# Kernel optimization log

Hardware: AMD Instinct MI355X
Metric: run time of the kernel (lower is better)

Reference implementation:

```python
import jax, jax.numpy as jnp
import numpy as np

BN_EPS = 1e-5


def binarize(x):
    # sign binarization with straight-through estimator (identity grad)
    return x + jax.lax.stop_gradient(jnp.sign(x) - x)


def conv2d(x, w, stride):
    # x: [N,C,H,W], w: [O,I,kh,kw], VALID padding (PyTorch default padding=0)
    return jax.lax.conv_general_dilated(
        x, w, window_strides=(stride, stride), padding='VALID',
        dimension_numbers=('NCHW', 'OIHW', 'NCHW'))


def batchnorm(x, gamma, beta, mean, var):
    inv = gamma / jnp.sqrt(var + BN_EPS)          # [C]
    return x * inv[None, :, None, None] + (beta - mean * inv)[None, :, None, None]


def setup_inputs() -> dict:
    key = jax.random.key(0)
    ks = jax.random.split(key, 20)
    B = 8192
    f32 = jnp.float32
    d = {
        'x': jax.random.normal(ks[0], (B, 1, 24, 54), f32),
        'conv1_w': jax.random.normal(ks[1], (32, 1, 3, 3), f32) * 0.3,
        'conv1_b': jax.random.normal(ks[2], (32,), f32) * 0.1,
        'bn1_gamma': 1.0 + 0.1 * jax.random.normal(ks[3], (32,), f32),
        'bn1_beta': 0.1 * jax.random.normal(ks[4], (32,), f32),
        'bn1_mean': 0.1 * jax.random.normal(ks[5], (32,), f32),
        'bn1_var': jax.random.uniform(ks[6], (32,), f32, 0.5, 1.5),
        'conv2_w': jax.random.normal(ks[7], (64, 32, 3, 3), f32) * 0.1,
        'conv2_b': jax.random.normal(ks[8], (64,), f32) * 0.1,
        'bn2_gamma': 1.0 + 0.1 * jax.random.normal(ks[9], (64,), f32),
        'bn2_beta': 0.1 * jax.random.normal(ks[10], (64,), f32),
        'bn2_mean': 0.1 * jax.random.normal(ks[11], (64,), f32),
        'bn2_var': jax.random.uniform(ks[12], (64,), f32, 0.5, 1.5),
        'lin_w': jax.random.normal(ks[13], (500, 3840), f32) * 0.02,
        'lin_b': jax.random.normal(ks[14], (500,), f32) * 0.1,
        'out_w': jax.random.normal(ks[15], (10, 500), f32) * 0.05,
        'out_b': jax.random.normal(ks[16], (10,), f32) * 0.1,
    }
    return d


def reference(x, conv1_w, conv1_b, bn1_gamma, bn1_beta, bn1_mean, bn1_var,
              conv2_w, conv2_b, bn2_gamma, bn2_beta, bn2_mean, bn2_var,
              lin_w, lin_b, out_w, out_b):
    # conv1: input channels (1) != 3 -> input binarized; weight binarized; float bias
    h = conv2d(binarize(x), binarize(conv1_w), 2) + conv1_b[None, :, None, None]
    h = jax.nn.relu(batchnorm(h, bn1_gamma, bn1_beta, bn1_mean, bn1_var))  # [B,32,11,26]
    # conv2: input channels (32) != 3 -> input binarized (values in {0,1} post-ReLU)
    h = conv2d(binarize(h), binarize(conv2_w), 2) + conv2_b[None, :, None, None]
    h = jax.nn.relu(batchnorm(h, bn2_gamma, bn2_beta, bn2_mean, bn2_var))  # [B,64,5,12]
    h = h.reshape(-1, 3840)
    # BinarizeLinear: in_features (3840, 500) != 784 -> input binarized
    h = jax.nn.relu(binarize(h) @ binarize(lin_w).T + lin_b[None, :])      # [B,500]
    y = binarize(h) @ binarize(out_w).T + out_b[None, :]                   # [B,10]
    return y
```

## Files before the change

### kernel.cpp

```cpp
#include <hip/hip_runtime.h>
#include <cstdint>

#define BN_EPS 1e-5f

static constexpr int NB = 8192;
static constexpr int JLIN = 500;


__global__ __launch_bounds__(256) void pack_kernel(
    const float* __restrict__ conv1_w, const float* __restrict__ conv1_b,
    const float* __restrict__ conv2_w, const float* __restrict__ conv2_b,
    const float* __restrict__ lin_w, const float* __restrict__ lin_b,
    const float* __restrict__ out_w,
    const float* __restrict__ bn1_g, const float* __restrict__ bn1_b,
    const float* __restrict__ bn1_m, const float* __restrict__ bn1_v,
    const float* __restrict__ bn2_g, const float* __restrict__ bn2_b,
    const float* __restrict__ bn2_m, const float* __restrict__ bn2_v,
    uint32_t* __restrict__ wlin4, uint32_t* __restrict__ cdat,
    uint32_t* __restrict__ lut, uint32_t* __restrict__ wout,
    int* __restrict__ Tlin)
{
    __shared__ uint32_t s_bm[122];
    __shared__ float    s_c1w[288];
    __shared__ uint32_t s_wp[32];
    __shared__ float    s_inv1[32], s_sh1[32], s_b1[32];

    int tid  = threadIdx.x;
    int lane = tid & 63;
    int wv   = tid >> 6;
    int b    = blockIdx.x;

    if (b < 500) {
        int j = b;
        if (tid == 0) { s_bm[120] = 0; s_bm[121] = 0; }
        for (int it = 0; it < 15; ++it) {
            int i = it * 256 + tid;
            float v = lin_w[(size_t)j * 3840 + i];
            uint64_t mask = __ballot(v > 0.0f);
            if (lane == 0)
                *((uint64_t*)&s_bm[(it * 256 + wv * 64) >> 5]) = mask;
        }
        __syncthreads();
        if (tid < 128) {
            int k = tid;
            int c = k >> 1, hi = k & 1;
            int nb = hi ? 28 : 32;
            int f0 = c * 60 + hi * 32;
            uint32_t lo  = s_bm[f0 >> 5];
            uint32_t hiw = s_bm[(f0 >> 5) + 1];
            int sh = f0 & 31;
            uint32_t word = (uint32_t)((((uint64_t)hiw << 32) | lo) >> sh);
            if (nb < 32) word &= (1u << nb) - 1u;
            int jw = j >> 6, jl = j & 63, kq = k >> 2, q = k & 3;
            wlin4[jw * 8192 + kq * 256 + jl * 4 + q] = word;
        }
        return;
    }

    int mb = b - 500;
    if (mb < 2) {
        for (int i = tid; i < 288; i += 256) s_c1w[i] = conv1_w[i];
        __syncthreads();
        if (tid < 32) {
            uint32_t wp = 0;
            for (int t = 0; t < 9; ++t)
                wp |= (s_c1w[tid * 9 + t] < 0.0f ? 1u : 0u) << t;
            s_wp[tid] = wp;
            float inv = bn1_g[tid] / sqrtf(bn1_v[tid] + BN_EPS);
            s_inv1[tid] = inv;
            s_sh1[tid]  = bn1_b[tid] - bn1_m[tid] * inv;
            s_b1[tid]   = conv1_b[tid];
        }
        __syncthreads();
        uint32_t px = (uint32_t)(mb * 256 + tid);
        uint32_t word = 0;
        for (int c = 0; c < 32; ++c) {
            int d = 9 - 2 * __popc(px ^ s_wp[c]);
            float z = __fadd_rn((float)d, s_b1[c]);
            z = __fadd_rn(__fmul_rn(z, s_inv1[c]), s_sh1[c]);
            word |= (z > 0.0f ? 1u : 0u) << c;
        }
        lut[px] = word;
        return;
    }

    int idx = (mb - 2) * 256 + tid;
    if (idx < 576) {
        int c = idx / 9, tap = idx % 9;
        uint32_t w = 0;
        for (int ic = 0; ic < 32; ++ic)
            w |= (conv2_w[c * 288 + ic * 9 + tap] > 0.0f ? 1u : 0u) << ic;
        float inv = bn2_g[c] / sqrtf(bn2_v[c] + BN_EPS);
        if (inv < 0.0f) w = ~w;
        cdat[tap * 64 + c] = w;
    } else if (idx < 576 + 64) {
        int c = idx - 576;
        float inv = bn2_g[c] / sqrtf(bn2_v[c] + BN_EPS);
        float sh  = bn2_b[c] - bn2_m[c] * inv;
        float b2  = conv2_b[c];
        int T = 10000;
        for (int u = -300; u <= 300; ++u) {
            float v = (inv < 0.0f) ? (float)(-u) : (float)u;
            float z = __fadd_rn(__fmul_rn(__fadd_rn(v, b2), inv), sh);
            if (z > 0.0f) { T = u; break; }
        }
        cdat[576 + c] = (uint32_t)T;
    } else if (idx < 576 + 64 + 512) {
        int j = idx - (576 + 64);
        int T = 10000;
        if (j < JLIN) {
            float lb = lin_b[j];
            int base = (int)floorf(-lb) - 2;
            for (int u = base; u <= base + 5; ++u)
                if (__fadd_rn((float)u, lb) > 0.0f) { T = u; break; }
        }
        Tlin[j] = T;
    } else if (idx < 576 + 64 + 512 + 160) {
        int t = idx - (576 + 64 + 512);
        int j = t >> 4, k = t & 15;
        uint32_t w = 0;
        for (int bb = 0; bb < 32; ++bb) {
            int jj = k * 32 + bb;
            if (jj < JLIN) w |= (out_w[j * 500 + jj] > 0.0f ? 1u : 0u) << bb;
        }
        wout[t] = w;
    }
}

__global__ __launch_bounds__(256) void conv_kernel(
    const float* __restrict__ x,
    const uint32_t* __restrict__ cdat,
    const uint32_t* __restrict__ lut,
    uint32_t* __restrict__ h2b, int* __restrict__ Bs)
{
    __shared__ __align__(8) uint32_t s_flat[4][44];
    __shared__ uint32_t s_lut[512];
    __shared__ __align__(8) uint32_t s_in[4][288];
    __shared__ uint32_t s_base[4][64];

    int tid  = threadIdx.x;
    int lane = tid & 63;
    int wv   = tid >> 6;
    int s    = blockIdx.x * 4 + wv;

    s_lut[tid]       = lut[tid];
    s_lut[tid + 256] = lut[tid + 256];

    const float* xs = x + (size_t)s * 1296;
    #pragma unroll
    for (int it = 0; it < 21; ++it) {
        int f = it * 64 + lane;
        float v = (f < 1296) ? xs[f] : 1.0f;
        uint64_t mk = __ballot(v < 0.0f);
        if (lane == 0) *((uint64_t*)&s_flat[wv][2 * it]) = mk;
    }
    __syncthreads();

    for (int i = tid; i < 4 * 286; i += 256) {
        int sl = i / 286, p = i - sl * 286;
        int oy = p / 26, ox = p - oy * 26;
        uint32_t pxb = 0;
        #pragma unroll
        for (int ky = 0; ky < 3; ++ky) {
            int bitpos = 54 * (2 * oy + ky) + 2 * ox;
            int d  = bitpos >> 5;
            int sh = bitpos & 31;
            uint64_t wp = (uint64_t)s_flat[sl][d] | ((uint64_t)s_flat[sl][d + 1] << 32);
            pxb |= (((uint32_t)(wp >> sh)) & 7u) << (3 * ky);
        }
        s_in[sl][p] = s_lut[pxb];
    }
    __syncthreads();

    for (int i = tid; i < 4 * 60; i += 256) {
        int sl = i / 60, p = i - sl * 60;
        int oy = p / 12, ox = p - 12 * oy;
        uint32_t sum = 0;
        #pragma unroll
        for (int ky = 0; ky < 3; ++ky) {
            const uint32_t* rp = &s_in[sl][(2 * oy + ky) * 26 + 2 * ox];
            sum += __popc(rp[0]) + __popc(rp[1]) + __popc(rp[2]);
        }
        s_base[sl][p] = sum;
    }
    __syncthreads();

    int c = lane;
    uint32_t m[9];
    #pragma unroll
    for (int q = 0; q < 9; ++q) m[q] = cdat[q * 64 + c];
    int T = (int)cdat[576 + c];

    uint64_t acc = 0;
    for (int oy = 0; oy < 5; ++oy) {
        int P[12];
        #pragma unroll
        for (int ox = 0; ox < 12; ++ox) P[ox] = 0;
        #pragma unroll
        for (int ky = 0; ky < 3; ++ky) {
            const uint32_t* rp = &s_in[wv][(2 * oy + ky) * 26];
            uint32_t r[25];
            #pragma unroll
            for (int d = 0; d < 12; ++d)
                *(uint64_t*)&r[2 * d] = *(const uint64_t*)&rp[2 * d];
            r[24] = rp[24];
            uint32_t m0 = m[ky * 3 + 0], m1 = m[ky * 3 + 1], m2 = m[ky * 3 + 2];
            #pragma unroll
            for (int ox = 0; ox < 12; ++ox) {
                P[ox] += __popc(r[2 * ox]     & m0);
                P[ox] += __popc(r[2 * ox + 1] & m1);
                P[ox] += __popc(r[2 * ox + 2] & m2);
            }
        }
        const uint32_t* bp = &s_base[wv][oy * 12];
        uint32_t bits = 0;
        #pragma unroll
        for (int ox = 0; ox < 12; ++ox) {
            int v = 2 * P[ox] - (int)bp[ox];
            bits |= (v >= T ? 1u : 0u) << ox;
        }
        acc |= (uint64_t)bits << (12 * oy);
    }
    uint32_t w0 = (uint32_t)acc;
    uint32_t w1 = (uint32_t)(acc >> 32) & 0x0FFFFFFFu;

    int bsum = __popc(w0) + __popc(w1);
    #pragma unroll
    for (int off = 32; off > 0; off >>= 1) bsum += __shfl_xor(bsum, off, 64);
    if (lane == 0) Bs[s] = bsum;

    *(uint2*)(h2b + (size_t)s * 128 + 2 * c) = make_uint2(w0, w1);
}

__global__ __launch_bounds__(256) void lin_kernel(
    const uint32_t* __restrict__ h2b,
    const uint32_t* __restrict__ wlin4,
    const int* __restrict__ Tlin,
    const int* __restrict__ Bs,
    const uint32_t* __restrict__ wout,
    const float* __restrict__ out_b,
    float* __restrict__ out)
{
    __shared__ uint4    s_w[2048];
    __shared__ uint64_t s_h3[16][8];
    __shared__ uint64_t s_wout[10][8];

    int tid  = threadIdx.x;
    int lane = tid & 63;
    int wv   = __builtin_amdgcn_readfirstlane((int)(tid >> 6));
    int sbase = blockIdx.x * 16;

    if (tid < 80) ((uint64_t*)s_wout)[tid] = ((const uint64_t*)wout)[tid];

    for (int jw = 0; jw < 8; ++jw) {
        const uint4* wsrc = (const uint4*)wlin4 + (size_t)jw * 2048;
        #pragma unroll
        for (int i = 0; i < 8; ++i)
            s_w[i * 256 + tid] = wsrc[i * 256 + tid];
        int T = Tlin[jw * 64 + lane];
        __syncthreads();

        int smp = sbase + wv * 4;
        int P[4] = {0, 0, 0, 0};
        #pragma unroll 4
        for (int kq = 0; kq < 32; ++kq) {
            uint4 w4 = s_w[kq * 64 + lane];
            #pragma unroll
            for (int i = 0; i < 4; ++i) {
                uint4 a = *((const uint4*)(h2b + (size_t)(smp + i) * 128) + kq);
                P[i] += __popc(a.x & w4.x);
                P[i] += __popc(a.y & w4.y);
                P[i] += __popc(a.z & w4.z);
                P[i] += __popc(a.w & w4.w);
            }
        }
        #pragma unroll
        for (int i = 0; i < 4; ++i) {
            int v = 2 * P[i] - Bs[smp + i];
            uint64_t mk = __ballot(v >= T);
            if (lane == 0) s_h3[wv * 4 + i][jw] = mk;
        }
        __syncthreads();
    }

    if (tid < 160) {
        int sl = tid / 10, o = tid - sl * 10;
        int P = 0, B = 0;
        #pragma unroll
        for (int k = 0; k < 8; ++k) {
            uint64_t a = s_h3[sl][k];
            P += __popcll(a & s_wout[o][k]);
            B += __popcll(a);
        }
        out[(size_t)(sbase + sl) * 10 + o] = __fadd_rn((float)(2 * P - B), out_b[o]);
    }
}

extern "C" void kernel_launch(void* const* d_in, const int* in_sizes, int n_in,
                              void* d_out, int out_size, void* d_ws, size_t ws_size,
                              hipStream_t stream)
{
    const float* x       = (const float*)d_in[0];
    const float* conv1_w = (const float*)d_in[1];
    const float* conv1_b = (const float*)d_in[2];
    const float* bn1_g   = (const float*)d_in[3];
    const float* bn1_b   = (const float*)d_in[4];
    const float* bn1_m   = (const float*)d_in[5];
    const float* bn1_v   = (const float*)d_in[6];
    const float* conv2_w = (const float*)d_in[7];
    const float* conv2_b = (const float*)d_in[8];
    const float* bn2_g   = (const float*)d_in[9];
    const float* bn2_b   = (const float*)d_in[10];
    const float* bn2_m   = (const float*)d_in[11];
    const float* bn2_v   = (const float*)d_in[12];
    const float* lin_w   = (const float*)d_in[13];
    const float* lin_b   = (const float*)d_in[14];
    const float* out_w   = (const float*)d_in[15];
    const float* out_b   = (const float*)d_in[16];

    char* ws = (char*)d_ws;
    uint32_t* h2b   = (uint32_t*)(ws + 0);
    uint32_t* wlin4 = (uint32_t*)(ws + 4718592);
    uint32_t* cdat  = (uint32_t*)(ws + 4980736);
    uint32_t* lut   = (uint32_t*)(ws + 4983296);
    uint32_t* wout  = (uint32_t*)(ws + 4985344);
    int*      Tlin  = (int*)     (ws + 4985984);
    int*      Bs    = (int*)     (ws + 4988032);

    pack_kernel<<<508, 256, 0, stream>>>(conv1_w, conv1_b, conv2_w, conv2_b,
                                         lin_w, lin_b, out_w,
                                         bn1_g, bn1_b, bn1_m, bn1_v,
                                         bn2_g, bn2_b, bn2_m, bn2_v,
                                         wlin4, cdat, lut, wout, Tlin);
    conv_kernel<<<NB / 4, 256, 0, stream>>>(x, cdat, lut, h2b, Bs);
    lin_kernel<<<512, 256, 0, stream>>>(h2b, wlin4, Tlin, Bs, wout, out_b,
                                        (float*)d_out);
}
```

Measured before the change: 199.6 us.

## Halve samples per linear block and pack linear weights per-thread with float4 loads

The linear kernel now handles 8 samples per block (2 per wave) instead of 16, doubling the grid to 1024 blocks for better occupancy and latency hiding. The cost is that each block re-stages the full packed weight matrix into LDS twice as often. Separately, the weight-packing stage drops the ballot-plus-shared-memory scheme and has each thread build one packed word directly from float4 loads. This shrinks that kernel's grid from 508 to 258 blocks but gives uncoalesced, strided reads.

```diff
diff --git a/kernel.cpp b/kernel.cpp
--- a/kernel.cpp
+++ b/kernel.cpp
@@ -20,44 +20,33 @@
     uint32_t* __restrict__ lut, uint32_t* __restrict__ wout,
     int* __restrict__ Tlin)
 {
-    __shared__ uint32_t s_bm[122];
     __shared__ float    s_c1w[288];
     __shared__ uint32_t s_wp[32];
     __shared__ float    s_inv1[32], s_sh1[32], s_b1[32];
 
-    int tid  = threadIdx.x;
-    int lane = tid & 63;
-    int wv   = tid >> 6;
-    int b    = blockIdx.x;
-
-    if (b < 500) {
-        int j = b;
-        if (tid == 0) { s_bm[120] = 0; s_bm[121] = 0; }
-        for (int it = 0; it < 15; ++it) {
-            int i = it * 256 + tid;
-            float v = lin_w[(size_t)j * 3840 + i];
-            uint64_t mask = __ballot(v > 0.0f);
-            if (lane == 0)
-                *((uint64_t*)&s_bm[(it * 256 + wv * 64) >> 5]) = mask;
-        }
-        __syncthreads();
-        if (tid < 128) {
-            int k = tid;
-            int c = k >> 1, hi = k & 1;
-            int nb = hi ? 28 : 32;
-            int f0 = c * 60 + hi * 32;
-            uint32_t lo  = s_bm[f0 >> 5];
-            uint32_t hiw = s_bm[(f0 >> 5) + 1];
-            int sh = f0 & 31;
-            uint32_t word = (uint32_t)((((uint64_t)hiw << 32) | lo) >> sh);
-            if (nb < 32) word &= (1u << nb) - 1u;
-            int jw = j >> 6, jl = j & 63, kq = k >> 2, q = k & 3;
-            wlin4[jw * 8192 + kq * 256 + jl * 4 + q] = word;
-        }
+    int tid = threadIdx.x;
+    int b   = blockIdx.x;
+
+    if (b < 250) {
+        int idx = b * 256 + tid;
+        int j = idx >> 7, k = idx & 127;
+        int c = k >> 1, hi = k & 1;
+        const float4* s4 = (const float4*)(lin_w + (size_t)j * 3840 + c * 60 + hi * 32);
+        int nq = hi ? 7 : 8;
+        uint32_t word = 0;
+        for (int qq = 0; qq < nq; ++qq) {
+            float4 v = s4[qq];
+            word |= (v.x > 0.0f ? 1u : 0u) << (4 * qq);
+            word |= (v.y > 0.0f ? 1u : 0u) << (4 * qq + 1);
+            word |= (v.z > 0.0f ? 1u : 0u) << (4 * qq + 2);
+            word |= (v.w > 0.0f ? 1u : 0u) << (4 * qq + 3);
+        }
+        int jw = j >> 6, jl = j & 63, kq = k >> 2, q = k & 3;
+        wlin4[jw * 8192 + kq * 256 + jl * 4 + q] = word;
         return;
     }
 
-    int mb = b - 500;
+    int mb = b - 250;
     if (mb < 2) {
         for (int i = tid; i < 288; i += 256) s_c1w[i] = conv1_w[i];
         __syncthreads();
@@ -242,15 +231,18 @@
     float* __restrict__ out)
 {
     __shared__ uint4    s_w[2048];
-    __shared__ uint64_t s_h3[16][8];
+    __shared__ uint64_t s_h3[8][8];
     __shared__ uint64_t s_wout[10][8];
 
     int tid  = threadIdx.x;
     int lane = tid & 63;
     int wv   = __builtin_amdgcn_readfirstlane((int)(tid >> 6));
-    int sbase = blockIdx.x * 16;
+    int sbase = blockIdx.x * 8;
 
     if (tid < 80) ((uint64_t*)s_wout)[tid] = ((const uint64_t*)wout)[tid];
+
+    int smp = sbase + wv * 2;
+    int B0 = Bs[smp], B1 = Bs[smp + 1];
 
     for (int jw = 0; jw < 8; ++jw) {
         const uint4* wsrc = (const uint4*)wlin4 + (size_t)jw * 2048;
@@ -260,30 +252,29 @@
         int T = Tlin[jw * 64 + lane];
         __syncthreads();
 
-        int smp = sbase + wv * 4;
-        int P[4] = {0, 0, 0, 0};
-        #pragma unroll 4
+        int P0 = 0, P1 = 0;
+        const uint4* a0p = (const uint4*)(h2b + (size_t)smp * 128);
+        const uint4* a1p = (const uint4*)(h2b + (size_t)(smp + 1) * 128);
+        #pragma unroll 8
         for (int kq = 0; kq < 32; ++kq) {
             uint4 w4 = s_w[kq * 64 + lane];
-            #pragma unroll
-            for (int i = 0; i < 4; ++i) {
-                uint4 a = *((const uint4*)(h2b + (size_t)(smp + i) * 128) + kq);
-                P[i] += __popc(a.x & w4.x);
-                P[i] += __popc(a.y & w4.y);
-                P[i] += __popc(a.z & w4.z);
-                P[i] += __popc(a.w & w4.w);
-            }
-        }
-        #pragma unroll
-        for (int i = 0; i < 4; ++i) {
-            int v = 2 * P[i] - Bs[smp + i];
-            uint64_t mk = __ballot(v >= T);
-            if (lane == 0) s_h3[wv * 4 + i][jw] = mk;
+            uint4 a0 = a0p[kq];
+            uint4 a1 = a1p[kq];
+            P0 += __popc(a0.x & w4.x); P1 += __popc(a1.x & w4.x);
+            P0 += __popc(a0.y & w4.y); P1 += __popc(a1.y & w4.y);
+            P0 += __popc(a0.z & w4.z); P1 += __popc(a1.z & w4.z);
+            P0 += __popc(a0.w & w4.w); P1 += __popc(a1.w & w4.w);
+        }
+        uint64_t mk0 = __ballot(2 * P0 >= T + B0);
+        uint64_t mk1 = __ballot(2 * P1 >= T + B1);
+        if (lane == 0) {
+            s_h3[wv * 2][jw]     = mk0;
+            s_h3[wv * 2 + 1][jw] = mk1;
         }
         __syncthreads();
     }
 
-    if (tid < 160) {
+    if (tid < 80) {
         int sl = tid / 10, o = tid - sl * 10;
         int P = 0, B = 0;
         #pragma unroll
@@ -327,12 +318,12 @@
     int*      Tlin  = (int*)     (ws + 4985984);
     int*      Bs    = (int*)     (ws + 4988032);
 
-    pack_kernel<<<508, 256, 0, stream>>>(conv1_w, conv1_b, conv2_w, conv2_b,
+    pack_kernel<<<258, 256, 0, stream>>>(conv1_w, conv1_b, conv2_w, conv2_b,
                                          lin_w, lin_b, out_w,
                                          bn1_g, bn1_b, bn1_m, bn1_v,
                                          bn2_g, bn2_b, bn2_m, bn2_v,
                                          wlin4, cdat, lut, wout, Tlin);
     conv_kernel<<<NB / 4, 256, 0, stream>>>(x, cdat, lut, h2b, Bs);
-    lin_kernel<<<512, 256, 0, stream>>>(h2b, wlin4, Tlin, Bs, wout, out_b,
-                                        (float*)d_out);
+    lin_kernel<<<1024, 256, 0, stream>>>(h2b, wlin4, Tlin, Bs, wout, out_b,
+                                         (float*)d_out);
 }
```

Result: slower. 204.1 us (+2.3%).
